# Performance work log

Measured on AMD Instinct MI355X. Metric: run time of the kernel, lower is better.

The kernel has to match this reference:

```python
import jax, jax.numpy as jnp
import numpy as np

VOCAB, EMBED, HIDDEN = 10000, 256, 512


def setup_inputs() -> dict:
    key = jax.random.key(0)
    ks = jax.random.split(key, 16)
    u = lambda k, shape, fan: jax.random.uniform(k, shape, jnp.float32) * np.sqrt(2.0 / fan)
    inp = {
        "input_": jax.random.randint(ks[0], (128, 64), 0, VOCAB, dtype=jnp.int64) if jax.config.jax_enable_x64 else jax.random.randint(ks[0], (128, 64), 0, VOCAB, dtype=jnp.int32),
        "embeddings": jax.random.normal(ks[1], (VOCAB, EMBED), jnp.float32),
        "W_xi": u(ks[2], (EMBED, HIDDEN), EMBED + HIDDEN),
        "W_hi": u(ks[3], (HIDDEN, HIDDEN), 2 * HIDDEN),
        "b_i": jax.random.uniform(ks[4], (1, HIDDEN), jnp.float32),
        "W_xf": u(ks[5], (EMBED, HIDDEN), EMBED + HIDDEN),
        "W_hf": u(ks[6], (HIDDEN, HIDDEN), 2 * HIDDEN),
        "b_f": jax.random.uniform(ks[7], (1, HIDDEN), jnp.float32),
        "W_xc": u(ks[8], (EMBED, HIDDEN), EMBED + HIDDEN),
        "W_hc": u(ks[9], (HIDDEN, HIDDEN), 2 * HIDDEN),
        "b_c": jax.random.uniform(ks[10], (1, HIDDEN), jnp.float32),
        "W_xo": u(ks[11], (EMBED, HIDDEN), EMBED + HIDDEN),
        "W_ho": u(ks[12], (HIDDEN, HIDDEN), 2 * HIDDEN),
        "b_o": jax.random.uniform(ks[13], (1, HIDDEN), jnp.float32),
        "W": u(ks[14], (HIDDEN, VOCAB), HIDDEN + VOCAB),
        "b": jax.random.uniform(ks[15], (1, VOCAB), jnp.float32),
    }
    return inp


def reference(input_, embeddings, W_xi, W_hi, b_i, W_xf, W_hf, b_f,
              W_xc, W_hc, b_c, W_xo, W_ho, b_o, W, b):
    T, B = input_.shape
    H = W_hi.shape[0]
    embeds = embeddings[input_]  # [T, B, E]
    # Precompute input-to-gate projections for all timesteps (batched GEMMs)
    xi = jnp.einsum('tbe,eh->tbh', embeds, W_xi) + b_i
    xf = jnp.einsum('tbe,eh->tbh', embeds, W_xf) + b_f
    xc = jnp.einsum('tbe,eh->tbh', embeds, W_xc) + b_c
    xo = jnp.einsum('tbe,eh->tbh', embeds, W_xo) + b_o

    def step(carry, xs):
        h_t, c_t = carry
        xi_t, xf_t, xc_t, xo_t = xs
        i_t = jax.nn.sigmoid(xi_t + h_t @ W_hi)
        f_t = jax.nn.sigmoid(xf_t + h_t @ W_hf)
        g_t = jnp.tanh(xc_t + h_t @ W_hc)
        o_t = jax.nn.sigmoid(xo_t + h_t @ W_ho)
        c_t = f_t * c_t + i_t * g_t
        h_t = o_t * jnp.tanh(c_t)
        return (h_t, c_t), h_t

    h0 = jnp.zeros((B, H), jnp.float32)
    c0 = jnp.zeros((B, H), jnp.float32)
    (h_t, c_t), hs = jax.lax.scan(step, (h0, c0), (xi, xf, xc, xo))  # hs: [T, B, H]
    # Output projection batched over all timesteps, matching torch.cat(tmp, 0)
    output = hs.reshape(T * B, H) @ W + b  # [T*B, VOCAB]
    return output, (h_t, c_t)
```

## Files before the change

kernel.cpp:

```cpp
#include <hip/hip_runtime.h>
#include <stdint.h>

#define T_STEPS 128
#define BATCH   64
#define EMBED   256
#define HIDDEN  512
#define VOCAB   10000
#define M_ROWS  (T_STEPS*BATCH)
#define NGATE   (4*HIDDEN)
#define NBLK    32
#define NLAUNCH 256
#define NGEMM   (NLAUNCH-NBLK)
#define NTILE_N 125
#define NTILE_M 64

typedef __attribute__((ext_vector_type(2))) float  f32x2;
typedef __attribute__((ext_vector_type(4))) float  f32x4;
typedef __attribute__((ext_vector_type(4))) int    i32x4;
typedef __attribute__((ext_vector_type(8))) __bf16 bf16x8;

static __device__ __forceinline__ unsigned short f32_to_bf16(float f) {
    union { float f; uint32_t u; } v; v.f = f;
    uint32_t u = v.u;
    return (unsigned short)((u + 0x7FFFu + ((u >> 16) & 1u)) >> 16);
}
static __device__ __forceinline__ float sigf(float x) {
    return 1.f / (1.f + __expf(-x));
}
static __device__ __forceinline__ float tanhfast(float x) {
    float e = __expf(2.f * fminf(fmaxf(x, -15.f), 15.f));
    return (e - 1.f) / (e + 1.f);
}
static __device__ __forceinline__ void cell2(
    float pi0, float pi1, float pf0, float pf1, float pg0, float pg1,
    float po0, float po1, float& c0, float& c1, float& h0, float& h1) {
    float i0 = sigf(pi0), i1 = sigf(pi1);
    float f0 = sigf(pf0), f1 = sigf(pf1);
    float g0 = tanhfast(pg0), g1 = tanhfast(pg1);
    float o0 = sigf(po0), o1 = sigf(po1);
    c0 = f0 * c0 + i0 * g0;
    c1 = f1 * c1 + i1 * g1;
    h0 = o0 * tanhfast(c0);
    h1 = o1 * tanhfast(c1);
}

static __device__ __forceinline__ i32x4 ld16ic(const void* p) {
    i32x4 r; asm volatile("global_load_dwordx4 %0, %1, off sc0 sc1" : "=v"(r) : "v"(p)); return r;
}
static __device__ __forceinline__ unsigned ld4ic(const void* p) {
    unsigned r; asm volatile("global_load_dword %0, %1, off sc0 sc1" : "=v"(r) : "v"(p)); return r;
}
static __device__ __forceinline__ void st4ic(void* p, unsigned v) {
    asm volatile("global_store_dword %0, %1, off sc0 sc1" :: "v"(p), "v"(v) : "memory");
}

__global__ void prep0(const float* __restrict__ E, unsigned short* __restrict__ Eb,
                      unsigned* __restrict__ hs, unsigned* __restrict__ fl) {
    size_t t = (size_t)blockIdx.x * 256 + threadIdx.x;
    size_t i = t * 4;
    if (i < (size_t)VOCAB * EMBED) {
        f32x4 v = *reinterpret_cast<const f32x4*>(E + i);
        unsigned short o[4];
        #pragma unroll
        for (int j = 0; j < 4; ++j) o[j] = f32_to_bf16(v[j]);
        *reinterpret_cast<unsigned long long*>(Eb + i) =
            ((unsigned long long)o[3] << 48) | ((unsigned long long)o[2] << 32) |
            ((unsigned long long)o[1] << 16) | (unsigned long long)o[0];
    }
    if (t < 524288) {
        i32x4 v = { -1, -1, -1, -1 };
        asm volatile("global_store_dwordx4 %0, %1, off sc0 sc1"
                     :: "v"((char*)hs + t * 16), "v"(v) : "memory");
    }
    if (t < 2048) {
        i32x4 z = { 0, 0, 0, 0 };
        asm volatile("global_store_dwordx4 %0, %1, off sc0 sc1"
                     :: "v"((char*)fl + t * 16), "v"(z) : "memory");
    }
}

__global__ void wt_convert(const float* __restrict__ W, unsigned short* __restrict__ Wt) {
    __shared__ float tile[32][33];
    int n0 = blockIdx.x * 32;
    int k0 = blockIdx.y * 32;
    int tx = threadIdx.x, ty = threadIdx.y;
    int n = n0 + tx;
    if (n < VOCAB) tile[ty][tx] = W[(size_t)(k0 + ty) * VOCAB + n];
    __syncthreads();
    int nn = n0 + ty;
    if (nn < VOCAB) Wt[(size_t)nn * HIDDEN + k0 + tx] = f32_to_bf16(tile[tx][ty]);
}

__global__ void wh_convert(const float* __restrict__ Whi, const float* __restrict__ Whf,
                           const float* __restrict__ Whc, const float* __restrict__ Who,
                           unsigned short* __restrict__ WhT) {
    __shared__ float tile[32][33];
    int g = blockIdx.z;
    const float* Wg = (g == 0) ? Whi : (g == 1) ? Whf : (g == 2) ? Whc : Who;
    int n0 = blockIdx.x * 32, k0 = blockIdx.y * 32;
    int tx = threadIdx.x, ty = threadIdx.y;
    tile[ty][tx] = Wg[(size_t)(k0 + ty) * HIDDEN + n0 + tx];
    __syncthreads();
    WhT[((size_t)g * HIDDEN + n0 + ty) * HIDDEN + k0 + tx] = f32_to_bf16(tile[tx][ty]);
}

__global__ void wx_convert(const float* __restrict__ Wxi, const float* __restrict__ Wxf,
                           const float* __restrict__ Wxc, const float* __restrict__ Wxo,
                           unsigned short* __restrict__ WxT) {
    __shared__ float tile[32][33];
    int g = blockIdx.z;
    const float* Wg = (g == 0) ? Wxi : (g == 1) ? Wxf : (g == 2) ? Wxc : Wxo;
    int n0 = blockIdx.x * 32, k0 = blockIdx.y * 32;
    int tx = threadIdx.x, ty = threadIdx.y;
    tile[ty][tx] = Wg[(size_t)(k0 + ty) * HIDDEN + n0 + tx];
    __syncthreads();
    WxT[((size_t)g * HIDDEN + n0 + ty) * EMBED + k0 + tx] = f32_to_bf16(tile[tx][ty]);
}

__global__ __launch_bounds__(256) void xproj_mfma(
    const int* __restrict__ idx, const unsigned short* __restrict__ Eb,
    const unsigned short* __restrict__ WxT,
    const float* __restrict__ bi,  const float* __restrict__ bf_,
    const float* __restrict__ bc,  const float* __restrict__ bo,
    float* __restrict__ xg)
{
    __shared__ __align__(16) char sA[128 * 128];
    __shared__ __align__(16) char sB[64 * 128];
    int n0 = blockIdx.x * 64;
    int m0 = blockIdx.y * 128;
    int tid = threadIdx.x;
    int w = tid >> 6, lane = tid & 63;
    f32x4 acc[2][4] = {};

    int arow[4], aer[4];
    #pragma unroll
    for (int i = 0; i < 4; ++i) {
        int s = tid + i * 256;
        arow[i] = s >> 3;
        aer[i]  = idx[m0 + arow[i]];
    }

    for (int kc = 0; kc < 4; ++kc) {
        int k0 = kc * 64;
        #pragma unroll
        for (int i = 0; i < 4; ++i) {
            int s = tid + i * 256;
            int row = arow[i], slot = s & 7;
            i32x4 v = *reinterpret_cast<const i32x4*>(Eb + (size_t)aer[i] * EMBED + k0 + slot * 8);
            *reinterpret_cast<i32x4*>(sA + row * 128 + ((slot ^ (row & 7)) * 16)) = v;
        }
        #pragma unroll
        for (int i = 0; i < 2; ++i) {
            int s = tid + i * 256;
            int row = s >> 3, slot = s & 7;
            i32x4 v = *reinterpret_cast<const i32x4*>(WxT + (size_t)(n0 + row) * EMBED + k0 + slot * 8);
            *reinterpret_cast<i32x4*>(sB + row * 128 + ((slot ^ (row & 7)) * 16)) = v;
        }
        __syncthreads();
        #pragma unroll
        for (int k2 = 0; k2 < 2; ++k2) {
            bf16x8 a[2], b[4];
            #pragma unroll
            for (int rf = 0; rf < 2; ++rf) {
                int row = w * 32 + rf * 16 + (lane & 15);
                int off = (k2 * 64 + (lane >> 4) * 16) ^ ((row & 7) << 4);
                a[rf] = *reinterpret_cast<const bf16x8*>(sA + row * 128 + off);
            }
            #pragma unroll
            for (int cf = 0; cf < 4; ++cf) {
                int row = cf * 16 + (lane & 15);
                int off = (k2 * 64 + (lane >> 4) * 16) ^ ((row & 7) << 4);
                b[cf] = *reinterpret_cast<const bf16x8*>(sB + row * 128 + off);
            }
            #pragma unroll
            for (int rf = 0; rf < 2; ++rf)
                #pragma unroll
                for (int cf = 0; cf < 4; ++cf)
                    acc[rf][cf] = __builtin_amdgcn_mfma_f32_16x16x32_bf16(a[rf], b[cf], acc[rf][cf], 0, 0, 0);
        }
        __syncthreads();
    }
    #pragma unroll
    for (int cf = 0; cf < 4; ++cf) {
        int col = n0 + cf * 16 + (lane & 15);
        int g = col >> 9, hc = col & 511;
        const float* bg = (g == 0) ? bi : (g == 1) ? bf_ : (g == 2) ? bc : bo;
        float bv = bg[hc];
        #pragma unroll
        for (int rf = 0; rf < 2; ++rf)
            #pragma unroll
            for (int r = 0; r < 4; ++r) {
                int row = m0 + w * 32 + rf * 16 + (lane >> 4) * 4 + r;
                xg[(size_t)row * NGATE + col] = acc[rf][cf][r] + bv;
            }
    }
}

__global__ __launch_bounds__(512) void lstm_fused(
    const float* __restrict__ xg,
    const unsigned short* __restrict__ WhT,
    unsigned short* hsbf,
    float* __restrict__ outp,
    const unsigned short* __restrict__ Btbf,
    const float* __restrict__ bias,
    float* __restrict__ Cout,
    unsigned* flags)
{
    __shared__ __align__(16) unsigned char smem[41472];
    const int tid = threadIdx.x;

    if (blockIdx.x < NBLK) {
        unsigned char* hstage = smem;
        auto P_lds = reinterpret_cast<float (*)[32][17]>(smem + 32768);
        const int bx   = blockIdx.x;
        const int hc0  = bx * 16;
        const int lane = tid & 63, w = tid >> 6;
        const int wm   = w >> 2, wg = w & 3;

        bf16x8 breg[16];
        {
            const unsigned short* base =
                WhT + ((size_t)wg * HIDDEN + hc0 + (lane & 15)) * HIDDEN + (lane >> 4) * 8;
            #pragma unroll
            for (int ks = 0; ks < 16; ++ks)
                breg[ks] = *reinterpret_cast<const bf16x8*>(base + ks * 32);
        }

        const int ub  = tid >> 3;
        const int uhp = tid & 7;
        const int uhc = hc0 + uhp * 2;
        float cA0 = 0.f, cA1 = 0.f, cB0 = 0.f, cB1 = 0.f;
        f32x2 xvA[4], xvB[4];
        if (tid < 256) {
            const float* xrA = xg + (size_t)(0 * 32 + ub) * NGATE + uhc;
            const float* xrB = xg + (size_t)(1 * 32 + ub) * NGATE + uhc;
            #pragma unroll
            for (int g = 0; g < 4; ++g) {
                xvA[g] = *reinterpret_cast<const f32x2*>(xrA + g * HIDDEN);
                xvB[g] = *reinterpret_cast<const f32x2*>(xrB + g * HIDDEN);
            }
        }
        unsigned* hs32 = reinterpret_cast<unsigned*>(hsbf);

#define CHK(R) { mx = (mx > (unsigned)R[0]) ? mx : (unsigned)R[0]; \
                 mx = (mx > (unsigned)R[1]) ? mx : (unsigned)R[1]; \
                 mx = (mx > (unsigned)R[2]) ? mx : (unsigned)R[2]; \
                 mx = (mx > (unsigned)R[3]) ? mx : (unsigned)R[3]; }
#define STLDS(R, I) { int s16 = (I) * 512 + tid; int row = s16 >> 6, sl = s16 & 63; \
        *reinterpret_cast<i32x4*>(hstage + row * 1024 + ((sl ^ (row & 7)) << 4)) = R; }

#define GROUP_UPDATE(G, XV, C0, C1, TT)                                         \
    if (tid < 256) {                                                            \
        int hp2 = uhp * 2;                                                      \
        float h0, h1;                                                           \
        cell2(P_lds[0][ub][hp2] + XV[0][0], P_lds[0][ub][hp2+1] + XV[0][1],     \
              P_lds[1][ub][hp2] + XV[1][0], P_lds[1][ub][hp2+1] + XV[1][1],     \
              P_lds[2][ub][hp2] + XV[2][0], P_lds[2][ub][hp2+1] + XV[2][1],     \
              P_lds[3][ub][hp2] + XV[3][0], P_lds[3][ub][hp2+1] + XV[3][1],     \
              C0, C1, h0, h1);                                                  \
        unsigned hp = ((unsigned)f32_to_bf16(h1) << 16) | (unsigned)f32_to_bf16(h0); \
        st4ic(hs32 + (size_t)(TT) * 16384 + ((G) * 32 + ub) * 256 + (uhc >> 1), hp); \
        if ((TT) == T_STEPS - 1) {                                              \
            f32x2 hv = { h0, h1 };                                              \
            *reinterpret_cast<f32x2*>(outp + (size_t)((G) * 32 + ub) * HIDDEN + uhc) = hv; \
            f32x2 cv = { C0, C1 };                                              \
            *reinterpret_cast<f32x2*>(outp + 32768 + (size_t)((G) * 32 + ub) * HIDDEN + uhc) = cv; \
        } else {                                                                \
            const float* xr = xg + (size_t)(((TT) + 1) * BATCH + (G) * 32 + ub) * NGATE + uhc; \
            _Pragma("unroll")                                                   \
            for (int g = 0; g < 4; ++g)                                         \
                XV[g] = *reinterpret_cast<const f32x2*>(xr + g * HIDDEN);       \
        }                                                                       \
    }

#define GROUP_PHASE(G, XV, C0, C1, TT)                                          \
    {                                                                           \
        f32x4 acc = {0.f, 0.f, 0.f, 0.f};                                       \
        {                                                                       \
            const char* hb = (const char*)hsbf + (size_t)((TT) - 1) * 65536 + (G) * 32768; \
            i32x4 q0, q1, q2, q3;                                               \
            for (int rnd = 0; rnd < (1 << 16); ++rnd) {                         \
                q0 = ld16ic(hb + (size_t)(0 * 512 + tid) * 16);                 \
                q1 = ld16ic(hb + (size_t)(1 * 512 + tid) * 16);                 \
                q2 = ld16ic(hb + (size_t)(2 * 512 + tid) * 16);                 \
                q3 = ld16ic(hb + (size_t)(3 * 512 + tid) * 16);                 \
                asm volatile("s_waitcnt vmcnt(0)"                               \
                    : "+v"(q0), "+v"(q1), "+v"(q2), "+v"(q3));                  \
                unsigned mx = 0u;                                               \
                CHK(q0) CHK(q1) CHK(q2) CHK(q3)                                 \
                if (mx != 0xFFFFFFFFu) break;                                   \
                __builtin_amdgcn_s_sleep(1);                                    \
            }                                                                   \
            __builtin_amdgcn_sched_barrier(0);                                  \
            STLDS(q0, 0) STLDS(q1, 1) STLDS(q2, 2) STLDS(q3, 3)                 \
        }                                                                       \
        __syncthreads();     \
        if (tid == 0) {                                                         \
            int s_ = 2 * (TT) + (G);                                            \
            int ps = s_ - 1;                                                    \
            st4ic(flags + ((size_t)(ps >> 1) * 64 + (ps & 1) * 32 + bx), 1u);   \
            if (s_ == 2) st4ic(flags + bx, 1u);             \
        }                                                                       \
        {                                                                       \
            const int rr = wm * 16 + (lane & 15);                               \
            _Pragma("unroll")                                                   \
            for (int ks = 0; ks < 16; ++ks) {                                   \
                int sl = ks * 4 + (lane >> 4);                                  \
                bf16x8 a = *reinterpret_cast<const bf16x8*>(                    \
                    hstage + rr * 1024 + ((sl ^ (rr & 7)) << 4));               \
                acc = __builtin_amdgcn_mfma_f32_16x16x32_bf16(a, breg[ks], acc, 0, 0, 0); \
            }                                                                   \
        }                                                                       \
        {                                                                       \
            int colr = lane & 15, rowb = (lane >> 4) * 4;                       \
            _Pragma("unroll")                                                   \
            for (int r = 0; r < 4; ++r)                                         \
                P_lds[wg][wm * 16 + rowb + r][colr] = acc[r];                   \
        }                                                                       \
        __syncthreads();                                                        \
        GROUP_UPDATE(G, XV, C0, C1, TT)                                         \
    }

        if (tid < 256) {
            float h0, h1;
            cell2(xvA[0][0], xvA[0][1], xvA[1][0], xvA[1][1],
                  xvA[2][0], xvA[2][1], xvA[3][0], xvA[3][1], cA0, cA1, h0, h1);
            unsigned hp = ((unsigned)f32_to_bf16(h1) << 16) | (unsigned)f32_to_bf16(h0);
            st4ic(hs32 + (size_t)(0 * 32 + ub) * 256 + (uhc >> 1), hp);
            const float* xr = xg + (size_t)(1 * BATCH + 0 * 32 + ub) * NGATE + uhc;
            #pragma unroll
            for (int g = 0; g < 4; ++g)
                xvA[g] = *reinterpret_cast<const f32x2*>(xr + g * HIDDEN);

            cell2(xvB[0][0], xvB[0][1], xvB[1][0], xvB[1][1],
                  xvB[2][0], xvB[2][1], xvB[3][0], xvB[3][1], cB0, cB1, h0, h1);
            hp = ((unsigned)f32_to_bf16(h1) << 16) | (unsigned)f32_to_bf16(h0);
            st4ic(hs32 + (size_t)(1 * 32 + ub) * 256 + (uhc >> 1), hp);
            xr = xg + (size_t)(1 * BATCH + 1 * 32 + ub) * NGATE + uhc;
            #pragma unroll
            for (int g = 0; g < 4; ++g)
                xvB[g] = *reinterpret_cast<const f32x2*>(xr + g * HIDDEN);
        }

        for (int t = 1; t < T_STEPS; ++t) {
            GROUP_PHASE(0, xvA, cA0, cA1, t)
            GROUP_PHASE(1, xvB, cB0, cB1, t)
        }
#undef GROUP_PHASE
#undef GROUP_UPDATE
#undef STLDS
#undef CHK
        __syncthreads();
        if (tid == 0)
            st4ic(flags + ((size_t)127 * 64 + 32 + bx), 1u);
    } else {
        char* sA = (char*)smem;
        char* sB = (char*)smem + 16384;
        const int gbid = blockIdx.x - NBLK;
        const int w = tid >> 6, lane = tid & 63;
        const unsigned short* __restrict__ Abf = hsbf;

        int ni, mi_lo, mi_hi;
        if (gbid < 99)       { ni = gbid;       mi_lo = 0;  mi_hi = 32; }
        else if (gbid < 125) { ni = gbid;       mi_lo = 0;  mi_hi = 64; }
        else                 { ni = gbid - 125; mi_lo = 32; mi_hi = 64; }
        const int n0 = ni * 80;

        const int ar0 = tid >> 3, ar1 = (tid >> 3) + 64, aslot = tid & 7;
        const int br0 = tid >> 3, bs0 = tid & 7;
        const int br1 = (512 + tid) >> 3, bs1 = tid & 7;

        for (int mi = mi_lo; mi < mi_hi; ++mi) {
            int m0 = mi * 128;
            {
                const unsigned* fl = flags + (size_t)2 * mi * 64;
                for (int rnd = 0; rnd < (1 << 20); ++rnd) {
                    unsigned v = 1u;
                    if (tid < 128) v = ld4ic(fl + tid);
                    asm volatile("s_waitcnt vmcnt(0)" : "+v"(v));
                    int bad = (tid < 128) && (v == 0u);
                    if (__syncthreads_count(bad) == 0) break;
                    __builtin_amdgcn_s_sleep(16);
                }
                asm volatile("" ::: "memory");
            }
            f32x4 acc[5] = {};
            i32x4 ra0, ra1, rb0, rb1;
            {
                ra0 = *reinterpret_cast<const i32x4*>(Abf + (size_t)(m0 + ar0) * HIDDEN + aslot * 8);
                ra1 = *reinterpret_cast<const i32x4*>(Abf + (size_t)(m0 + ar1) * HIDDEN + aslot * 8);
                rb0 = *reinterpret_cast<const i32x4*>(Btbf + (size_t)(n0 + br0) * HIDDEN + bs0 * 8);
                if (tid < 128)
                    rb1 = *reinterpret_cast<const i32x4*>(Btbf + (size_t)(n0 + br1) * HIDDEN + bs1 * 8);
            }
            for (int kc = 0; kc < 8; ++kc) {
                *reinterpret_cast<i32x4*>(sA + ar0 * 128 + ((aslot ^ (ar0 & 7)) * 16)) = ra0;
                *reinterpret_cast<i32x4*>(sA + ar1 * 128 + ((aslot ^ (ar1 & 7)) * 16)) = ra1;
                *reinterpret_cast<i32x4*>(sB + br0 * 128 + ((bs0 ^ (br0 & 7)) * 16)) = rb0;
                if (tid < 128)
                    *reinterpret_cast<i32x4*>(sB + br1 * 128 + ((bs1 ^ (br1 & 7)) * 16)) = rb1;
                __syncthreads();
                if (kc < 7) {
                    int k1 = (kc + 1) * 64;
                    ra0 = *reinterpret_cast<const i32x4*>(Abf + (size_t)(m0 + ar0) * HIDDEN + k1 + aslot * 8);
                    ra1 = *reinterpret_cast<const i32x4*>(Abf + (size_t)(m0 + ar1) * HIDDEN + k1 + aslot * 8);
                    rb0 = *reinterpret_cast<const i32x4*>(Btbf + (size_t)(n0 + br0) * HIDDEN + k1 + bs0 * 8);
                    if (tid < 128)
                        rb1 = *reinterpret_cast<const i32x4*>(Btbf + (size_t)(n0 + br1) * HIDDEN + k1 + bs1 * 8);
                }
                #pragma unroll
                for (int k2 = 0; k2 < 2; ++k2) {
                    int arow = w * 16 + (lane & 15);
                    int aoff = (k2 * 64 + (lane >> 4) * 16) ^ ((arow & 7) << 4);
                    bf16x8 a = *reinterpret_cast<const bf16x8*>(sA + arow * 128 + aoff);
                    #pragma unroll
                    for (int cf = 0; cf < 5; ++cf) {
                        int brow = cf * 16 + (lane & 15);
                        int boff = (k2 * 64 + (lane >> 4) * 16) ^ ((brow & 7) << 4);
                        bf16x8 b = *reinterpret_cast<const bf16x8*>(sB + brow * 128 + boff);
                        acc[cf] = __builtin_amdgcn_mfma_f32_16x16x32_bf16(a, b, acc[cf], 0, 0, 0);
                    }
                }
                __syncthreads();
            }
            #pragma unroll
            for (int cf = 0; cf < 5; ++cf) {
                int col = n0 + cf * 16 + (lane & 15);
                float bv = bias[col];
                #pragma unroll
                for (int r = 0; r < 4; ++r) {
                    int row = m0 + w * 16 + (lane >> 4) * 4 + r;
                    Cout[(size_t)row * VOCAB + col] = acc[cf][r] + bv;
                }
            }
        }
    }
}

extern "C" void kernel_launch(void* const* d_in, const int* in_sizes, int n_in,
                              void* d_out, int out_size, void* d_ws, size_t ws_size,
                              hipStream_t stream) {
    (void)in_sizes; (void)n_in; (void)out_size; (void)ws_size;
    const int*   input_ = (const int*)  d_in[0];
    const float* Emb    = (const float*)d_in[1];
    const float* Wxi    = (const float*)d_in[2];
    const float* Whi    = (const float*)d_in[3];
    const float* bi     = (const float*)d_in[4];
    const float* Wxf    = (const float*)d_in[5];
    const float* Whf    = (const float*)d_in[6];
    const float* bf_    = (const float*)d_in[7];
    const float* Wxc    = (const float*)d_in[8];
    const float* Whc    = (const float*)d_in[9];
    const float* bc     = (const float*)d_in[10];
    const float* Wxo    = (const float*)d_in[11];
    const float* Who    = (const float*)d_in[12];
    const float* bo     = (const float*)d_in[13];
    const float* W      = (const float*)d_in[14];
    const float* b      = (const float*)d_in[15];
    float* out = (float*)d_out;

    char* ws = (char*)d_ws;
    float*          xg   = (float*)         (ws);
    unsigned short* hsbf = (unsigned short*)(ws +  67108864);
    unsigned short* Wtbf = (unsigned short*)(ws +  75497472);
    unsigned short* WhT  = (unsigned short*)(ws +  85737472);
    unsigned short* Embb = (unsigned short*)(ws +  87834624);
    unsigned short* WxT  = (unsigned short*)(ws +  92954624);
    unsigned*       flags= (unsigned*)      (ws +  94003200);

    prep0<<<2500, 256, 0, stream>>>(Emb, Embb, (unsigned*)hsbf, flags);
    wt_convert<<<dim3(313, 16), dim3(32, 32), 0, stream>>>(W, Wtbf);
    wh_convert<<<dim3(16, 16, 4), dim3(32, 32), 0, stream>>>(Whi, Whf, Whc, Who, WhT);
    wx_convert<<<dim3(16, 8, 4), dim3(32, 32), 0, stream>>>(Wxi, Wxf, Wxc, Wxo, WxT);
    xproj_mfma<<<dim3(32, 64), 256, 0, stream>>>(input_, Embb, WxT, bi, bf_, bc, bo, xg);

    {
        const float* xg_c = xg;
        const unsigned short* WhT_c = WhT;
        unsigned short* hsbf_p = hsbf;
        float* outp = out + (size_t)M_ROWS * VOCAB;
        const unsigned short* Wtbf_c = Wtbf;
        const float* b_c = b;
        float* out_p = out;
        unsigned* flags_p = flags;
        void* args[] = { (void*)&xg_c, (void*)&WhT_c, (void*)&hsbf_p,
                         (void*)&outp,
                         (void*)&Wtbf_c, (void*)&b_c, (void*)&out_p, (void*)&flags_p };
        hipLaunchCooperativeKernel((void*)lstm_fused, dim3(NLAUNCH), dim3(512), args, 0, stream);
    }
}
```

Baseline: 600.8 us.

## Merge prep kernels and convert output weights inside GEMM blocks during recurrence

Folds the embedding conversion, flag and hidden-state initialisation, and the recurrent and input weight transposes into one prep launch. The output-projection weight transpose and bf16 conversion moves into the idle GEMM blocks of the cooperative LSTM kernel, so it overlaps the serial recurrence, gated by an atomic counter barrier. Output stores become non-temporal. This removes several launches and pulls the W conversion off the critical path, at the cost of an extra intra-kernel barrier among the GEMM blocks and a wt_ctr counter that must start at zero (it falls inside the flag range prep clears).

```diff
diff --git a/kernel.cpp b/kernel.cpp
--- a/kernel.cpp
+++ b/kernel.cpp
@@ -53,68 +53,63 @@
 static __device__ __forceinline__ void st4ic(void* p, unsigned v) {
     asm volatile("global_store_dword %0, %1, off sc0 sc1" :: "v"(p), "v"(v) : "memory");
 }
-
-__global__ void prep0(const float* __restrict__ E, unsigned short* __restrict__ Eb,
-                      unsigned* __restrict__ hs, unsigned* __restrict__ fl) {
-    size_t t = (size_t)blockIdx.x * 256 + threadIdx.x;
-    size_t i = t * 4;
-    if (i < (size_t)VOCAB * EMBED) {
-        f32x4 v = *reinterpret_cast<const f32x4*>(E + i);
-        unsigned short o[4];
-        #pragma unroll
-        for (int j = 0; j < 4; ++j) o[j] = f32_to_bf16(v[j]);
-        *reinterpret_cast<unsigned long long*>(Eb + i) =
-            ((unsigned long long)o[3] << 48) | ((unsigned long long)o[2] << 32) |
-            ((unsigned long long)o[1] << 16) | (unsigned long long)o[0];
-    }
-    if (t < 524288) {
-        i32x4 v = { -1, -1, -1, -1 };
-        asm volatile("global_store_dwordx4 %0, %1, off sc0 sc1"
-                     :: "v"((char*)hs + t * 16), "v"(v) : "memory");
-    }
-    if (t < 2048) {
-        i32x4 z = { 0, 0, 0, 0 };
-        asm volatile("global_store_dwordx4 %0, %1, off sc0 sc1"
-                     :: "v"((char*)fl + t * 16), "v"(z) : "memory");
-    }
-}
-
-__global__ void wt_convert(const float* __restrict__ W, unsigned short* __restrict__ Wt) {
+static __device__ __forceinline__ void st4nt(void* p, float v) {
+    asm volatile("global_store_dword %0, %1, off nt" :: "v"(p), "v"(v) : "memory");
+}
+
+__global__ __launch_bounds__(1024) void prep_all(
+    const float* __restrict__ E, unsigned short* __restrict__ Eb,
+    unsigned* __restrict__ hs, unsigned* __restrict__ fl,
+    const float* __restrict__ Whi, const float* __restrict__ Whf,
+    const float* __restrict__ Whc, const float* __restrict__ Who,
+    unsigned short* __restrict__ WhT,
+    const float* __restrict__ Wxi, const float* __restrict__ Wxf,
+    const float* __restrict__ Wxc, const float* __restrict__ Wxo,
+    unsigned short* __restrict__ WxT)
+{
     __shared__ float tile[32][33];
-    int n0 = blockIdx.x * 32;
-    int k0 = blockIdx.y * 32;
-    int tx = threadIdx.x, ty = threadIdx.y;
-    int n = n0 + tx;
-    if (n < VOCAB) tile[ty][tx] = W[(size_t)(k0 + ty) * VOCAB + n];
-    __syncthreads();
-    int nn = n0 + ty;
-    if (nn < VOCAB) Wt[(size_t)nn * HIDDEN + k0 + tx] = f32_to_bf16(tile[tx][ty]);
-}
-
-__global__ void wh_convert(const float* __restrict__ Whi, const float* __restrict__ Whf,
-                           const float* __restrict__ Whc, const float* __restrict__ Who,
-                           unsigned short* __restrict__ WhT) {
-    __shared__ float tile[32][33];
-    int g = blockIdx.z;
-    const float* Wg = (g == 0) ? Whi : (g == 1) ? Whf : (g == 2) ? Whc : Who;
-    int n0 = blockIdx.x * 32, k0 = blockIdx.y * 32;
-    int tx = threadIdx.x, ty = threadIdx.y;
-    tile[ty][tx] = Wg[(size_t)(k0 + ty) * HIDDEN + n0 + tx];
-    __syncthreads();
-    WhT[((size_t)g * HIDDEN + n0 + ty) * HIDDEN + k0 + tx] = f32_to_bf16(tile[tx][ty]);
-}
-
-__global__ void wx_convert(const float* __restrict__ Wxi, const float* __restrict__ Wxf,
-                           const float* __restrict__ Wxc, const float* __restrict__ Wxo,
-                           unsigned short* __restrict__ WxT) {
-    __shared__ float tile[32][33];
-    int g = blockIdx.z;
-    const float* Wg = (g == 0) ? Wxi : (g == 1) ? Wxf : (g == 2) ? Wxc : Wxo;
-    int n0 = blockIdx.x * 32, k0 = blockIdx.y * 32;
-    int tx = threadIdx.x, ty = threadIdx.y;
-    tile[ty][tx] = Wg[(size_t)(k0 + ty) * HIDDEN + n0 + tx];
-    __syncthreads();
-    WxT[((size_t)g * HIDDEN + n0 + ty) * EMBED + k0 + tx] = f32_to_bf16(tile[tx][ty]);
+    const int bid = blockIdx.x, tid = threadIdx.x;
+    if (bid < 625) {
+        size_t t = (size_t)bid * 1024 + tid;
+        size_t i = t * 4;
+        if (i < (size_t)VOCAB * EMBED) {
+            f32x4 v = *reinterpret_cast<const f32x4*>(E + i);
+            unsigned short o[4];
+            #pragma unroll
+            for (int j = 0; j < 4; ++j) o[j] = f32_to_bf16(v[j]);
+            *reinterpret_cast<unsigned long long*>(Eb + i) =
+                ((unsigned long long)o[3] << 48) | ((unsigned long long)o[2] << 32) |
+                ((unsigned long long)o[1] << 16) | (unsigned long long)o[0];
+        }
+        if (t < 524288) {
+            i32x4 v = { -1, -1, -1, -1 };
+            asm volatile("global_store_dwordx4 %0, %1, off sc0 sc1"
+                         :: "v"((char*)hs + t * 16), "v"(v) : "memory");
+        }
+        if (t < 2052) {
+            i32x4 z = { 0, 0, 0, 0 };
+            asm volatile("global_store_dwordx4 %0, %1, off sc0 sc1"
+                         :: "v"((char*)fl + t * 16), "v"(z) : "memory");
+        }
+    } else if (bid < 625 + 1024) {
+        int e = bid - 625;
+        int g = e >> 8, rem = e & 255;
+        int n0 = (rem >> 4) * 32, k0 = (rem & 15) * 32;
+        const float* Wg = (g == 0) ? Whi : (g == 1) ? Whf : (g == 2) ? Whc : Who;
+        int tx = tid & 31, ty = tid >> 5;
+        tile[ty][tx] = Wg[(size_t)(k0 + ty) * HIDDEN + n0 + tx];
+        __syncthreads();
+        WhT[((size_t)g * HIDDEN + n0 + ty) * HIDDEN + k0 + tx] = f32_to_bf16(tile[tx][ty]);
+    } else {
+        int e = bid - 1649;
+        int g = e >> 7, rem = e & 127;
+        int n0 = (rem >> 3) * 32, k0 = (rem & 7) * 32;
+        const float* Wg = (g == 0) ? Wxi : (g == 1) ? Wxf : (g == 2) ? Wxc : Wxo;
+        int tx = tid & 31, ty = tid >> 5;
+        tile[ty][tx] = Wg[(size_t)(k0 + ty) * HIDDEN + n0 + tx];
+        __syncthreads();
+        WxT[((size_t)g * HIDDEN + n0 + ty) * EMBED + k0 + tx] = f32_to_bf16(tile[tx][ty]);
+    }
 }
 
 __global__ __launch_bounds__(256) void xproj_mfma(
@@ -201,10 +196,12 @@
     const unsigned short* __restrict__ WhT,
     unsigned short* hsbf,
     float* __restrict__ outp,
-    const unsigned short* __restrict__ Btbf,
+    unsigned short* Wtbf,
+    const float* __restrict__ Wf,
     const float* __restrict__ bias,
     float* __restrict__ Cout,
-    unsigned* flags)
+    unsigned* flags,
+    unsigned* wt_ctr)
 {
     __shared__ __align__(16) unsigned char smem[41472];
     const int tid = threadIdx.x;
@@ -354,11 +351,60 @@
         if (tid == 0)
             st4ic(flags + ((size_t)127 * 64 + 32 + bx), 1u);
     } else {
+        const int gbid = blockIdx.x - NBLK;
+        const int w = tid >> 6, lane = tid & 63;
+        {
+            auto tl = reinterpret_cast<float (*)[68]>(smem);
+            for (int tix = gbid; tix < 157 * 8; tix += NGEMM) {
+                int kt = tix / 157, nt_ = tix - kt * 157;
+                int n0c = nt_ * 64, k0c = kt * 64;
+                #pragma unroll
+                for (int i = 0; i < 2; ++i) {
+                    int u = tid + i * 512;
+                    int kk = u >> 4, n4 = u & 15;
+                    int nn = n0c + n4 * 4;
+                    if (nn + 3 < VOCAB) {
+                        f32x4 v = *reinterpret_cast<const f32x4*>(
+                            Wf + (size_t)(k0c + kk) * VOCAB + nn);
+                        *reinterpret_cast<f32x4*>(&tl[kk][n4 * 4]) = v;
+                    }
+                }
+                __syncthreads();
+                {
+                    int n = tid >> 3, u8 = tid & 7;
+                    if (n0c + n < VOCAB) {
+                        unsigned short o[8];
+                        #pragma unroll
+                        for (int j = 0; j < 8; ++j) o[j] = f32_to_bf16(tl[u8 * 8 + j][n]);
+                        i32x4 pk;
+                        pk[0] = (int)(o[0] | ((unsigned)o[1] << 16));
+                        pk[1] = (int)(o[2] | ((unsigned)o[3] << 16));
+                        pk[2] = (int)(o[4] | ((unsigned)o[5] << 16));
+                        pk[3] = (int)(o[6] | ((unsigned)o[7] << 16));
+                        asm volatile("global_store_dwordx4 %0, %1, off sc0 sc1"
+                            :: "v"(Wtbf + (size_t)(n0c + n) * HIDDEN + k0c + u8 * 8),
+                               "v"(pk) : "memory");
+                    }
+                }
+                __syncthreads();
+            }
+            asm volatile("s_waitcnt vmcnt(0)" ::: "memory");
+            __syncthreads();
+            if (tid == 0) {
+                __hip_atomic_fetch_add(wt_ctr, 1u, __ATOMIC_RELAXED, __HIP_MEMORY_SCOPE_AGENT);
+                for (int rnd = 0; rnd < (1 << 20); ++rnd) {
+                    unsigned v = ld4ic(wt_ctr);
+                    asm volatile("s_waitcnt vmcnt(0)" : "+v"(v));
+                    if (v >= (unsigned)NGEMM) break;
+                    __builtin_amdgcn_s_sleep(8);
+                }
+            }
+            __syncthreads();
+        }
         char* sA = (char*)smem;
         char* sB = (char*)smem + 16384;
-        const int gbid = blockIdx.x - NBLK;
-        const int w = tid >> 6, lane = tid & 63;
         const unsigned short* __restrict__ Abf = hsbf;
+        const unsigned short* __restrict__ Btbf = Wtbf;
 
         int ni, mi_lo, mi_hi;
         if (gbid < 99)       { ni = gbid;       mi_lo = 0;  mi_hi = 32; }
@@ -430,7 +476,7 @@
                 #pragma unroll
                 for (int r = 0; r < 4; ++r) {
                     int row = m0 + w * 16 + (lane >> 4) * 4 + r;
-                    Cout[(size_t)row * VOCAB + col] = acc[cf][r] + bv;
+                    st4nt(&Cout[(size_t)row * VOCAB + col], acc[cf][r] + bv);
                 }
             }
         }
@@ -467,11 +513,11 @@
     unsigned short* Embb = (unsigned short*)(ws +  87834624);
     unsigned short* WxT  = (unsigned short*)(ws +  92954624);
     unsigned*       flags= (unsigned*)      (ws +  94003200);
-
-    prep0<<<2500, 256, 0, stream>>>(Emb, Embb, (unsigned*)hsbf, flags);
-    wt_convert<<<dim3(313, 16), dim3(32, 32), 0, stream>>>(W, Wtbf);
-    wh_convert<<<dim3(16, 16, 4), dim3(32, 32), 0, stream>>>(Whi, Whf, Whc, Who, WhT);
-    wx_convert<<<dim3(16, 8, 4), dim3(32, 32), 0, stream>>>(Wxi, Wxf, Wxc, Wxo, WxT);
+    unsigned*       wtc  = (unsigned*)      (ws +  94035968);
+
+    prep_all<<<2161, 1024, 0, stream>>>(Emb, Embb, (unsigned*)hsbf, flags,
+                                        Whi, Whf, Whc, Who, WhT,
+                                        Wxi, Wxf, Wxc, Wxo, WxT);
     xproj_mfma<<<dim3(32, 64), 256, 0, stream>>>(input_, Embb, WxT, bi, bf_, bc, bo, xg);
 
     {
@@ -479,13 +525,15 @@
         const unsigned short* WhT_c = WhT;
         unsigned short* hsbf_p = hsbf;
         float* outp = out + (size_t)M_ROWS * VOCAB;
-        const unsigned short* Wtbf_c = Wtbf;
+        unsigned short* Wtbf_p = Wtbf;
+        const float* W_c = W;
         const float* b_c = b;
         float* out_p = out;
         unsigned* flags_p = flags;
+        unsigned* wtc_p = wtc;
         void* args[] = { (void*)&xg_c, (void*)&WhT_c, (void*)&hsbf_p,
-                         (void*)&outp,
-                         (void*)&Wtbf_c, (void*)&b_c, (void*)&out_p, (void*)&flags_p };
+                         (void*)&outp, (void*)&Wtbf_p, (void*)&W_c,
+                         (void*)&b_c, (void*)&out_p, (void*)&flags_p, (void*)&wtc_p };
         hipLaunchCooperativeKernel((void*)lstm_fused, dim3(NLAUNCH), dim3(512), args, 0, stream);
     }
 }
```

Measured after the change: 580.8 us. 3.3% less time.
